# Kernel optimization log

Measured on AMD Instinct MI355X. Metric: run time of the kernel, lower is better.

## Reference

```python
import jax, jax.numpy as jnp
import numpy as np

B, D, H, O, E = 16384, 1024, 512, 256, 8


def setup_inputs() -> dict:
    key = jax.random.key(0)
    ks = jax.random.split(key, 8)
    s = lambda k, shape, fan: (jax.random.normal(k, shape, jnp.float32) / np.sqrt(fan).astype(np.float32))
    z = lambda shape: jnp.zeros(shape, jnp.float32)
    return {
        "x": jax.random.normal(ks[0], (B, D), jnp.float32),
        # gating network: D -> 256 -> 128 -> E
        "gw1": s(ks[1], (D, 256), D), "gb1": z((256,)),
        "gw2": s(ks[2], (256, 128), 256), "gb2": z((128,)),
        "gw3": s(ks[3], (128, E), 128), "gb3": z((E,)),
        # experts, batched over expert dim E: D -> H -> H -> O
        "ew1": s(ks[4], (E, D, H), D), "eb1": z((E, H)),
        "ew2": s(ks[5], (E, H, H), H), "eb2": z((E, H)),
        "ew3": s(ks[6], (E, H, O), H), "eb3": z((E, O)),
    }


def reference(x, gw1, gb1, gw2, gb2, gw3, gb3, ew1, eb1, ew2, eb2, ew3, eb3):
    # Gating network (dropout is identity in eval mode)
    g = jax.nn.relu(x @ gw1 + gb1)
    g = jax.nn.relu(g @ gw2 + gb2)
    gates = jax.nn.softmax(g @ gw3 + gb3, axis=1)  # [B, E]
    # All experts run on every token: batched small MLPs over expert axis e
    h = jax.nn.relu(jnp.einsum('bd,edh->ebh', x, ew1) + eb1[:, None, :])   # [E, B, H]
    h = jax.nn.relu(jnp.einsum('ebh,ehk->ebk', h, ew2) + eb2[:, None, :])  # [E, B, H]
    eo = jnp.einsum('ebh,eho->ebo', h, ew3) + eb3[:, None, :]              # [E, B, O]
    # gate-weighted sum over experts
    out = jnp.einsum('ebo,be->bo', eo, gates)  # [B, O]
    return out
```

## Files before the change

kernel.cpp:

```cpp
#include <hip/hip_runtime.h>
#include <hip/hip_bf16.h>

typedef __hip_bfloat16 bf16;
typedef __attribute__((ext_vector_type(8))) __bf16 bf16x8;
typedef __attribute__((ext_vector_type(4))) float f32x4;

#define B_ 16384
#define D_ 1024
#define H_ 512
#define O_ 256
#define E_ 8
#define BC_ 8192

#define GLDS(src, dst) __builtin_amdgcn_global_load_lds( \
    (const __attribute__((address_space(1))) void*)(src), \
    (__attribute__((address_space(3))) void*)(dst), 16, 0, 0)

__global__ void detect_k(const unsigned short* __restrict__ x, int* __restrict__ flag) {
    __shared__ int s;
    if (threadIdx.x == 0) s = 0;
    __syncthreads();
    int big = 0;
    for (int i = threadIdx.x; i < 2048; i += 256)
        if (((x[i] >> 7) & 0xFF) >= 150) big = 1;
    if (big) atomicOr(&s, 1);
    __syncthreads();
    if (threadIdx.x == 0) *flag = s;
}

__global__ void cvt_k(const void* __restrict__ src, bf16* __restrict__ dst,
                      const int* __restrict__ flag, long n) {
    const int f = *flag;
    long i = (long)blockIdx.x * blockDim.x + threadIdx.x;
    const long stride = (long)gridDim.x * blockDim.x;
    if (f) {
        const float* s = (const float*)src;
        for (; i < n; i += stride) dst[i] = __float2bfloat16(s[i]);
    } else {
        const bf16* s = (const bf16*)src;
        for (; i < n; i += stride) dst[i] = s[i];
    }
}

__global__ void transpose_k(const void* __restrict__ in, bf16* __restrict__ out,
                            const int* __restrict__ flag, int R, int C) {
    __shared__ bf16 t[32][33];
    const int f = *flag;
    const long zo = (long)blockIdx.z * R * C;
    const int x = blockIdx.x * 32 + threadIdx.x;
    const int y0 = blockIdx.y * 32;
    const float* inf = (const float*)in;
    const bf16* inb = (const bf16*)in;
#pragma unroll
    for (int i = 0; i < 4; i++) {
        int r = y0 + threadIdx.y + i * 8;
        long idx = zo + (long)r * C + x;
        t[threadIdx.y + i * 8][threadIdx.x] =
            f ? __float2bfloat16(inf[idx]) : inb[idx];
    }
    __syncthreads();
    const int xr = blockIdx.y * 32 + threadIdx.x;
#pragma unroll
    for (int i = 0; i < 4; i++) {
        int c = blockIdx.x * 32 + threadIdx.y + i * 8;
        out[zo + (long)c * R + xr] = t[threadIdx.x][threadIdx.y + i * 8];
    }
}

__global__ void gate3_softmax_k(const bf16* __restrict__ g2,
                                const bf16* __restrict__ gw3,
                                const bf16* __restrict__ gb3,
                                float* __restrict__ gates) {
    __shared__ float w[128 * 8];
    __shared__ float bsh[8];
    const int tid = threadIdx.x;
    for (int i = tid; i < 1024; i += 256) w[i] = __bfloat162float(gw3[i]);
    if (tid < 8) bsh[tid] = __bfloat162float(gb3[tid]);
    __syncthreads();

    const long row = (long)blockIdx.x * 256 + tid;
    float acc[8];
#pragma unroll
    for (int o = 0; o < 8; o++) acc[o] = bsh[o];

    const bf16x8* rp8 = (const bf16x8*)(g2 + row * 128);
#pragma unroll 4
    for (int c8 = 0; c8 < 16; c8++) {
        bf16x8 v8 = rp8[c8];
#pragma unroll
        for (int jj = 0; jj < 8; jj++) {
            float v = (float)v8[jj];
            int k = c8 * 8 + jj;
#pragma unroll
            for (int o = 0; o < 8; o++) acc[o] += v * w[k * 8 + o];
        }
    }
    float m = acc[0];
#pragma unroll
    for (int o = 1; o < 8; o++) m = fmaxf(m, acc[o]);
    float s = 0.f;
#pragma unroll
    for (int o = 0; o < 8; o++) { acc[o] = __expf(acc[o] - m); s += acc[o]; }
    const float inv = 1.f / s;
#pragma unroll
    for (int o = 0; o < 8; o++) gates[row * 8 + o] = acc[o] * inv;
}

template <int MODE>
__global__ __launch_bounds__(256, 4)
void gemm_bt(const bf16* __restrict__ A, const bf16* __restrict__ Bt,
             const bf16* __restrict__ bias, const float* __restrict__ gates,
             void* __restrict__ Cout, const bf16* __restrict__ eb3,
             const int* __restrict__ oflag,
             int lda, int ldb, int ldo, int K,
             long a_z, long b_z, long bias_z, long out_z,
             int e_gate, int k_per_e, long a_e, long b_e, long row0) {
    __shared__ __attribute__((aligned(16))) bf16 As[128 * 32];
    __shared__ __attribute__((aligned(16))) bf16 Bs[128 * 32];

    const int tid  = threadIdx.x;
    const int lane = tid & 63;
    const int quad = lane >> 4;
    const int l15  = lane & 15;
    const int wid  = tid >> 6;
    const int wr   = (wid >> 1) << 6;
    const int wc   = (wid & 1) << 6;
    const int z    = blockIdx.z;
    const long m0  = (long)blockIdx.y << 7;
    const long n0  = (long)blockIdx.x << 7;

    const bf16* Az = A + (long)z * a_z;
    const bf16* Bz = Bt + (long)z * b_z;

    f32x4 acc[4][4];
#pragma unroll
    for (int i = 0; i < 4; i++)
#pragma unroll
        for (int j = 0; j < 4; j++) acc[i][j] = (f32x4){0.f, 0.f, 0.f, 0.f};

    const int erow = tid >> 2;
    const int ecol = (tid & 3) << 3;

    const int n_e   = k_per_e ? (K / k_per_e) : 1;
    const int inner = (k_per_e ? k_per_e : K) >> 5;

    for (int e = 0; e < n_e; e++) {
        const bf16* Ae = Az + (long)e * a_e;
        const bf16* Be = Bz + (long)e * b_e;
        for (int kti = 0; kti < inner; kti++) {
            const int kk = kti << 5;
#pragma unroll
            for (int i = 0; i < 2; i++) {
                const int r = (i << 6) + erow;
                GLDS(Ae + (m0 + r) * lda + (kk + ecol), As + r * 32 + ecol);
            }
#pragma unroll
            for (int i = 0; i < 2; i++) {
                const int r = (i << 6) + erow;
                GLDS(Be + (n0 + r) * ldb + (kk + ecol), Bs + r * 32 + ecol);
            }
            __syncthreads();
            bf16x8 af[4], bfr[4];
#pragma unroll
            for (int i = 0; i < 4; i++)
                af[i] = *(const bf16x8*)(As + (wr + i * 16 + l15) * 32 + (quad << 3));
#pragma unroll
            for (int j = 0; j < 4; j++)
                bfr[j] = *(const bf16x8*)(Bs + (wc + j * 16 + l15) * 32 + (quad << 3));
#pragma unroll
            for (int i = 0; i < 4; i++)
#pragma unroll
                for (int j = 0; j < 4; j++)
                    acc[i][j] = __builtin_amdgcn_mfma_f32_16x16x32_bf16(
                        af[i], bfr[j], acc[i][j], 0, 0, 0);
            __syncthreads();
        }
    }

    const int eg = (e_gate >= 0) ? e_gate : z;

    if constexpr (MODE == 0 || MODE == 1) {
        bf16* C = (bf16*)Cout + (long)z * out_z;
        const bf16* bb = bias + (long)z * bias_z;
        float gv[4][4];
        if constexpr (MODE == 1) {
#pragma unroll
            for (int i = 0; i < 4; i++)
#pragma unroll
                for (int rg = 0; rg < 4; rg++)
                    gv[i][rg] = gates[(row0 + m0 + wr + i * 16 + quad * 4 + rg) * 8 + eg];
        }
#pragma unroll
        for (int j = 0; j < 4; j++) {
            const int c = (int)n0 + wc + j * 16 + l15;
            const float bv = __bfloat162float(bb[c]);
#pragma unroll
            for (int i = 0; i < 4; i++) {
#pragma unroll
                for (int rg = 0; rg < 4; rg++) {
                    const long r = m0 + wr + i * 16 + quad * 4 + rg;
                    float v = fmaxf(acc[i][j][rg] + bv, 0.f);
                    if constexpr (MODE == 1) v *= gv[i][rg];
                    C[r * ldo + c] = __float2bfloat16(v);
                }
            }
        }
    } else if constexpr (MODE == 2) {
        float* C = (float*)Cout;
#pragma unroll
        for (int i = 0; i < 4; i++) {
#pragma unroll
            for (int rg = 0; rg < 4; rg++) {
                const long r = m0 + wr + i * 16 + quad * 4 + rg;
                const float g = gates[(row0 + r) * 8 + eg];
#pragma unroll
                for (int j = 0; j < 4; j++) {
                    const int c = (int)n0 + wc + j * 16 + l15;
                    const float b3 = __bfloat162float(eb3[eg * O_ + c]);
                    C[r * ldo + c] += acc[i][j][rg] + g * b3;
                }
            }
        }
    } else {
        float* C = (float*)Cout + (long)z * out_z;
        const int e0 = z * 2;
        float b30[4], b31[4];
#pragma unroll
        for (int j = 0; j < 4; j++) {
            const int c = (int)n0 + wc + j * 16 + l15;
            b30[j] = __bfloat162float(eb3[e0 * O_ + c]);
            b31[j] = __bfloat162float(eb3[(e0 + 1) * O_ + c]);
        }
#pragma unroll
        for (int i = 0; i < 4; i++) {
#pragma unroll
            for (int rg = 0; rg < 4; rg++) {
                const long r = m0 + wr + i * 16 + quad * 4 + rg;
                const float g0 = gates[(row0 + r) * 8 + e0];
                const float g1 = gates[(row0 + r) * 8 + e0 + 1];
#pragma unroll
                for (int j = 0; j < 4; j++) {
                    const int c = (int)n0 + wc + j * 16 + l15;
                    C[(row0 + r) * ldo + c] =
                        acc[i][j][rg] + g0 * b30[j] + g1 * b31[j];
                }
            }
        }
    }
}

__global__ void zero_f32_k(float* __restrict__ p) {
    p[(long)blockIdx.x * 256 + threadIdx.x] = 0.f;
}
__global__ void out_cvt_k(const float* __restrict__ in, void* __restrict__ out,
                          const int* __restrict__ flag) {
    const long i = (long)blockIdx.x * 256 + threadIdx.x;
    if (*flag) ((float*)out)[i] = in[i];
    else       ((bf16*)out)[i] = __float2bfloat16(in[i]);
}
__global__ void reduce4_k(const float* __restrict__ p, void* __restrict__ out,
                          const int* __restrict__ flag) {
    const long n = (long)B_ * O_;
    const long i = ((long)blockIdx.x * 256 + threadIdx.x) * 4;
    float4 a = *(const float4*)(p + i);
    float4 b = *(const float4*)(p + n + i);
    float4 c = *(const float4*)(p + 2 * n + i);
    float4 d = *(const float4*)(p + 3 * n + i);
    float4 s = {a.x + b.x + c.x + d.x, a.y + b.y + c.y + d.y,
                a.z + b.z + c.z + d.z, a.w + b.w + c.w + d.w};
    if (*flag) {
        *(float4*)((float*)out + i) = s;
    } else {
        bf16* o = (bf16*)out + i;
        o[0] = __float2bfloat16(s.x); o[1] = __float2bfloat16(s.y);
        o[2] = __float2bfloat16(s.z); o[3] = __float2bfloat16(s.w);
    }
}

extern "C" void kernel_launch(void* const* d_in, const int* in_sizes, int n_in,
                              void* d_out, int out_size, void* d_ws, size_t ws_size,
                              hipStream_t stream) {
    (void)in_sizes; (void)n_in; (void)out_size;
    const void* x   = d_in[0];
    const void* gw1 = d_in[1];
    const void* gb1 = d_in[2];
    const void* gw2 = d_in[3];
    const void* gb2 = d_in[4];
    const void* gw3 = d_in[5];
    const void* gb3 = d_in[6];
    const void* ew1 = d_in[7];
    const void* eb1 = d_in[8];
    const void* ew2 = d_in[9];
    const void* eb2 = d_in[10];
    const void* ew3 = d_in[11];
    const void* eb3 = d_in[12];

    char* ws = (char*)d_ws;
    size_t off = 0;
    auto alloc = [&](size_t n) { char* p = ws + off; off += (n + 255) & ~(size_t)255; return p; };

    int*  flag  = (int*)alloc(256);
    bf16* xc    = (bf16*)alloc((size_t)B_ * D_ * 2);
    bf16* gw1t  = (bf16*)alloc((size_t)256 * 1024 * 2);
    bf16* gw2t  = (bf16*)alloc((size_t)128 * 256 * 2);
    bf16* ew1t  = (bf16*)alloc((size_t)E_ * H_ * D_ * 2);
    bf16* ew2t  = (bf16*)alloc((size_t)E_ * H_ * H_ * 2);
    bf16* ew3t  = (bf16*)alloc((size_t)E_ * O_ * H_ * 2);
    bf16* gb1c  = (bf16*)alloc(256 * 2);
    bf16* gb2c  = (bf16*)alloc(128 * 2);
    bf16* gw3c  = (bf16*)alloc(1024 * 2);
    bf16* gb3c  = (bf16*)alloc(8 * 2);
    bf16* eb1c  = (bf16*)alloc((size_t)E_ * H_ * 2);
    bf16* eb2c  = (bf16*)alloc((size_t)E_ * H_ * 2);
    bf16* eb3c  = (bf16*)alloc((size_t)E_ * O_ * 2);
    bf16* g1    = (bf16*)alloc((size_t)B_ * 256 * 2);
    bf16* g2b   = (bf16*)alloc((size_t)B_ * 128 * 2);
    float* gates = (float*)alloc((size_t)B_ * 8 * 4);

    const size_t small = off;
    const size_t needA = small + 2ull * ((size_t)E_ * BC_ * H_ * 2 + 256)
                               + (4ull * B_ * O_ * 4 + 256) + 4096;
    const bool pathA = ws_size >= needA;

    detect_k<<<1, 256, 0, stream>>>((const unsigned short*)x, flag);

    cvt_k<<<4096, 256, 0, stream>>>(x, xc, flag, (long)B_ * D_);
    cvt_k<<<1, 256, 0, stream>>>(gb1, gb1c, flag, 256);
    cvt_k<<<1, 256, 0, stream>>>(gb2, gb2c, flag, 128);
    cvt_k<<<4, 256, 0, stream>>>(gw3, gw3c, flag, 1024);
    cvt_k<<<1, 256, 0, stream>>>(gb3, gb3c, flag, 8);
    cvt_k<<<16, 256, 0, stream>>>(eb1, eb1c, flag, (long)E_ * H_);
    cvt_k<<<16, 256, 0, stream>>>(eb2, eb2c, flag, (long)E_ * H_);
    cvt_k<<<8, 256, 0, stream>>>(eb3, eb3c, flag, (long)E_ * O_);

    transpose_k<<<dim3(256 / 32, 1024 / 32, 1), dim3(32, 8), 0, stream>>>(gw1, gw1t, flag, 1024, 256);
    transpose_k<<<dim3(128 / 32, 256 / 32, 1), dim3(32, 8), 0, stream>>>(gw2, gw2t, flag, 256, 128);
    transpose_k<<<dim3(H_ / 32, D_ / 32, E_), dim3(32, 8), 0, stream>>>(ew1, ew1t, flag, D_, H_);
    transpose_k<<<dim3(H_ / 32, H_ / 32, E_), dim3(32, 8), 0, stream>>>(ew2, ew2t, flag, H_, H_);
    transpose_k<<<dim3(O_ / 32, H_ / 32, E_), dim3(32, 8), 0, stream>>>(ew3, ew3t, flag, H_, O_);

    gemm_bt<0><<<dim3(2, 128, 1), 256, 0, stream>>>(
        xc, gw1t, gb1c, nullptr, g1, nullptr, nullptr,
        1024, 1024, 256, 1024, 0, 0, 0, 0, 0, 0, 0, 0, 0);
    gemm_bt<0><<<dim3(1, 128, 1), 256, 0, stream>>>(
        g1, gw2t, gb2c, nullptr, g2b, nullptr, nullptr,
        256, 256, 128, 256, 0, 0, 0, 0, 0, 0, 0, 0, 0);
    gate3_softmax_k<<<dim3(B_ / 256), 256, 0, stream>>>(g2b, gw3c, gb3c, gates);

    if (pathA) {
        bf16* h1c = (bf16*)alloc((size_t)E_ * BC_ * H_ * 2);
        bf16* h2c = (bf16*)alloc((size_t)E_ * BC_ * H_ * 2);
        float* parts = (float*)alloc(4ull * B_ * O_ * 4);
        for (int ci = 0; ci < B_ / BC_; ci++) {
            const long rb = (long)ci * BC_;
            gemm_bt<0><<<dim3(4, BC_ / 128, 8), 256, 0, stream>>>(
                xc + rb * D_, ew1t, eb1c, nullptr, h1c, nullptr, nullptr,
                D_, D_, H_, D_,
                0, (long)H_ * D_, H_, (long)BC_ * H_, 0, 0, 0, 0, 0);
            gemm_bt<1><<<dim3(4, BC_ / 128, 8), 256, 0, stream>>>(
                h1c, ew2t, eb2c, gates, h2c, nullptr, nullptr,
                H_, H_, H_, H_,
                (long)BC_ * H_, (long)H_ * H_, H_, (long)BC_ * H_, -1, 0, 0, 0, rb);
            gemm_bt<5><<<dim3(2, BC_ / 128, 4), 256, 0, stream>>>(
                h2c, ew3t, nullptr, gates, parts, eb3c, nullptr,
                H_, H_, O_, 1024,
                2L * BC_ * H_, 2L * O_ * H_, 0, (long)B_ * O_,
                2 , 512, (long)BC_ * H_, (long)O_ * H_, rb);
        }
        reduce4_k<<<dim3(B_ * O_ / 1024), 256, 0, stream>>>(parts, d_out, flag);
    } else {
        bf16* h1s = (bf16*)alloc((size_t)B_ * H_ * 2);
        bf16* h2s = (bf16*)alloc((size_t)B_ * H_ * 2);
        float* oacc = (float*)alloc((size_t)B_ * O_ * 4);
        zero_f32_k<<<dim3(B_ * O_ / 256), 256, 0, stream>>>(oacc);
        for (int e = 0; e < E_; e++) {
            gemm_bt<0><<<dim3(4, 128, 1), 256, 0, stream>>>(
                xc, ew1t + (size_t)e * H_ * D_, eb1c + (size_t)e * H_, nullptr, h1s, nullptr, nullptr,
                1024, 1024, 512, 1024, 0, 0, 0, 0, 0, 0, 0, 0, 0);
            gemm_bt<1><<<dim3(4, 128, 1), 256, 0, stream>>>(
                h1s, ew2t + (size_t)e * H_ * H_, eb2c + (size_t)e * H_, gates, h2s, nullptr, nullptr,
                512, 512, 512, 512, 0, 0, 0, 0, e, 0, 0, 0, 0);
            gemm_bt<2><<<dim3(2, 128, 1), 256, 0, stream>>>(
                h2s, ew3t + (size_t)e * O_ * H_, nullptr, gates, oacc, eb3c, nullptr,
                512, 512, 256, 512, 0, 0, 0, 0, e, 0, 0, 0, 0);
        }
        out_cvt_k<<<dim3(B_ * O_ / 256), 256, 0, stream>>>(oacc, d_out, flag);
    }
}
```

Baseline: 591.2 us.

## Double-buffer GEMM LDS tiles, swizzle LDS columns, fuse small conversion kernels

The GEMM main loop now uses two LDS buffers per operand. The next K-tile is prefetched with global_load_lds while MFMAs run on the current one, and one barrier per iteration replaces two. An XOR-style rotation of the 8-element column chunks is applied to both the stores and the fragment reads, to cut LDS bank conflicts. Seven tiny bias/weight conversion launches are merged into one kernel to reduce launch overhead. LDS use doubles to 32KB per block, which may reduce occupancy under the launch_bounds of 4 blocks per CU.

```diff
diff --git a/kernel.cpp b/kernel.cpp
--- a/kernel.cpp
+++ b/kernel.cpp
@@ -42,6 +42,21 @@
     }
 }
 
+__global__ void cvt_multi_k(const void* gb1, const void* gb2, const void* gw3,
+                            const void* gb3, const void* eb1, const void* eb2,
+                            const void* eb3,
+                            bf16* gb1c, bf16* gb2c, bf16* gw3c, bf16* gb3c,
+                            bf16* eb1c, bf16* eb2c, bf16* eb3c,
+                            const int* __restrict__ flag) {
+    const int f = *flag;
+    auto cv = [&](const void* s, bf16* d, int n) {
+        for (int i = threadIdx.x; i < n; i += 256)
+            d[i] = f ? __float2bfloat16(((const float*)s)[i]) : ((const bf16*)s)[i];
+    };
+    cv(gb1, gb1c, 256); cv(gb2, gb2c, 128); cv(gw3, gw3c, 1024); cv(gb3, gb3c, 8);
+    cv(eb1, eb1c, E_ * H_); cv(eb2, eb2c, E_ * H_); cv(eb3, eb3c, E_ * O_);
+}
+
 __global__ void transpose_k(const void* __restrict__ in, bf16* __restrict__ out,
                             const int* __restrict__ flag, int R, int C) {
     __shared__ bf16 t[32][33];
@@ -115,8 +130,8 @@
              int lda, int ldb, int ldo, int K,
              long a_z, long b_z, long bias_z, long out_z,
              int e_gate, int k_per_e, long a_e, long b_e, long row0) {
-    __shared__ __attribute__((aligned(16))) bf16 As[128 * 32];
-    __shared__ __attribute__((aligned(16))) bf16 Bs[128 * 32];
+    __shared__ __attribute__((aligned(16))) bf16 As[2 * 128 * 32];
+    __shared__ __attribute__((aligned(16))) bf16 Bs[2 * 128 * 32];
 
     const int tid  = threadIdx.x;
     const int lane = tid & 63;
@@ -138,43 +153,58 @@
 #pragma unroll
         for (int j = 0; j < 4; j++) acc[i][j] = (f32x4){0.f, 0.f, 0.f, 0.f};
 
-    const int erow = tid >> 2;
-    const int ecol = (tid & 3) << 3;
+    const int srow = tid >> 2;
+    const int scol = (((tid & 3) - (tid >> 3)) & 3) << 3;
+    const int dlt  = (((quad + (l15 >> 1)) & 3) << 3);
+
+    const long aoff0 = (m0 + srow) * lda + scol;
+    const long aoff1 = (m0 + 64 + srow) * lda + scol;
+    const long boff0 = (n0 + srow) * ldb + scol;
+    const long boff1 = (n0 + 64 + srow) * ldb + scol;
 
     const int n_e   = k_per_e ? (K / k_per_e) : 1;
     const int inner = (k_per_e ? k_per_e : K) >> 5;
-
-    for (int e = 0; e < n_e; e++) {
-        const bf16* Ae = Az + (long)e * a_e;
-        const bf16* Be = Bz + (long)e * b_e;
-        for (int kti = 0; kti < inner; kti++) {
-            const int kk = kti << 5;
-#pragma unroll
-            for (int i = 0; i < 2; i++) {
-                const int r = (i << 6) + erow;
-                GLDS(Ae + (m0 + r) * lda + (kk + ecol), As + r * 32 + ecol);
-            }
-#pragma unroll
-            for (int i = 0; i < 2; i++) {
-                const int r = (i << 6) + erow;
-                GLDS(Be + (n0 + r) * ldb + (kk + ecol), Bs + r * 32 + ecol);
-            }
-            __syncthreads();
-            bf16x8 af[4], bfr[4];
-#pragma unroll
-            for (int i = 0; i < 4; i++)
-                af[i] = *(const bf16x8*)(As + (wr + i * 16 + l15) * 32 + (quad << 3));
+    const int total = n_e * inner;
+
+    auto prefetch = [&](int buf, int e, int kti) {
+        const bf16* Ae = Az + (long)e * a_e + (kti << 5);
+        const bf16* Be = Bz + (long)e * b_e + (kti << 5);
+        bf16* as = As + (buf << 12);
+        bf16* bs = Bs + (buf << 12);
+        GLDS(Ae + aoff0, as + (tid << 3));
+        GLDS(Ae + aoff1, as + ((tid + 256) << 3));
+        GLDS(Be + boff0, bs + (tid << 3));
+        GLDS(Be + boff1, bs + ((tid + 256) << 3));
+    };
+
+    int pf_e = 0, pf_k = 0;
+    prefetch(0, 0, 0);
+    pf_k = 1;
+    __syncthreads();
+
+    for (int t = 0; t < total; t++) {
+        const int cur = t & 1;
+        if (t + 1 < total) {
+            prefetch(cur ^ 1, pf_e, pf_k);
+            pf_k++;
+            if (pf_k == inner) { pf_k = 0; pf_e++; }
+        }
+        const bf16* as = As + (cur << 12);
+        const bf16* bs = Bs + (cur << 12);
+        bf16x8 af[4], bfr[4];
+#pragma unroll
+        for (int i = 0; i < 4; i++)
+            af[i] = *(const bf16x8*)(as + (wr + i * 16 + l15) * 32 + dlt);
+#pragma unroll
+        for (int j = 0; j < 4; j++)
+            bfr[j] = *(const bf16x8*)(bs + (wc + j * 16 + l15) * 32 + dlt);
+#pragma unroll
+        for (int i = 0; i < 4; i++)
 #pragma unroll
             for (int j = 0; j < 4; j++)
-                bfr[j] = *(const bf16x8*)(Bs + (wc + j * 16 + l15) * 32 + (quad << 3));
-#pragma unroll
-            for (int i = 0; i < 4; i++)
-#pragma unroll
-                for (int j = 0; j < 4; j++)
-                    acc[i][j] = __builtin_amdgcn_mfma_f32_16x16x32_bf16(
-                        af[i], bfr[j], acc[i][j], 0, 0, 0);
-            __syncthreads();
-        }
+                acc[i][j] = __builtin_amdgcn_mfma_f32_16x16x32_bf16(
+                    af[i], bfr[j], acc[i][j], 0, 0, 0);
+        __syncthreads();
     }
 
     const int eg = (e_gate >= 0) ? e_gate : z;
@@ -325,13 +355,9 @@
     detect_k<<<1, 256, 0, stream>>>((const unsigned short*)x, flag);
 
     cvt_k<<<4096, 256, 0, stream>>>(x, xc, flag, (long)B_ * D_);
-    cvt_k<<<1, 256, 0, stream>>>(gb1, gb1c, flag, 256);
-    cvt_k<<<1, 256, 0, stream>>>(gb2, gb2c, flag, 128);
-    cvt_k<<<4, 256, 0, stream>>>(gw3, gw3c, flag, 1024);
-    cvt_k<<<1, 256, 0, stream>>>(gb3, gb3c, flag, 8);
-    cvt_k<<<16, 256, 0, stream>>>(eb1, eb1c, flag, (long)E_ * H_);
-    cvt_k<<<16, 256, 0, stream>>>(eb2, eb2c, flag, (long)E_ * H_);
-    cvt_k<<<8, 256, 0, stream>>>(eb3, eb3c, flag, (long)E_ * O_);
+    cvt_multi_k<<<1, 256, 0, stream>>>(gb1, gb2, gw3, gb3, eb1, eb2, eb3,
+                                       gb1c, gb2c, gw3c, gb3c, eb1c, eb2c, eb3c,
+                                       flag);
 
     transpose_k<<<dim3(256 / 32, 1024 / 32, 1), dim3(32, 8), 0, stream>>>(gw1, gw1t, flag, 1024, 256);
     transpose_k<<<dim3(128 / 32, 256 / 32, 1), dim3(32, 8), 0, stream>>>(gw2, gw2t, flag, 256, 128);
```

Result: no change. 594.5 us (+0.5%).
